# Kernel tuning notes

Hardware: AMD Instinct MI355X
Metric: run time of the kernel (lower is better)

## Reference

```python
import jax, jax.numpy as jnp
import numpy as np

N = 2500   # total_neurons
K = 50     # connections_per_neuron
T = 60     # temporal_sequence
F = 5      # input_features
H = 128    # lstm hidden_size
B = 512    # batch
GROUPS = [800, 700, 600, 400]  # support_resistance, trend_detection, pattern_recognition, volume_analysis


def _lstm_layer(x, Wih, Whh, bih, bhh):
    # x: [B, T, D]; PyTorch gate order (i, f, g, o); eval mode (no dropout)
    bs = x.shape[0]
    h0 = jnp.zeros((bs, H), x.dtype)

    def step(carry, xt):
        h, c = carry
        g = xt @ Wih.T + h @ Whh.T + bih + bhh
        i, f, gg, o = jnp.split(g, 4, axis=-1)
        c = jax.nn.sigmoid(f) * c + jax.nn.sigmoid(i) * jnp.tanh(gg)
        h = jax.nn.sigmoid(o) * jnp.tanh(c)
        return (h, c), h

    (h, c), ys = jax.lax.scan(step, (h0, h0), jnp.swapaxes(x, 0, 1))
    return jnp.swapaxes(ys, 0, 1), h


def _forward(x, W_ih0, W_hh0, b_ih0, b_hh0, W_ih1, W_hh1, b_ih1, b_hh1,
             fp_w1, fp_b1, fp_w2, fp_b2, conn_w, sens, thr,
             int_w1, int_b1, int_w2, int_b2, int_w3, int_b3,
             tw, tb, pw, pb, kw, kb, vw, vb, cw, cb, conn_idx):
    y0, _ = _lstm_layer(x, W_ih0, W_hh0, b_ih0, b_hh0)
    _, hlast = _lstm_layer(y0, W_ih1, W_hh1, b_ih1, b_hh1)        # hidden[-1]: [B, H]
    base = jnp.tanh(jax.nn.relu(hlast @ fp_w1.T + fp_b1) @ fp_w2.T + fp_b2)  # [B, 32]
    # all_activations = base repeated over N neurons; each neuron reduces its
    # K gathered activations (weighted) and the identical 32 feature dims to a scalar.
    feat_sum = base.sum(-1)                                        # [B]
    acts = jnp.broadcast_to(feat_sum[:, None], (x.shape[0], N))    # [B, N]
    gathered = acts[:, conn_idx]                                   # [B, N, K] irregular gather
    wi = jnp.einsum('bnk,nk->bn', gathered, conn_w)                # [B, N]
    pre = wi * sens
    o0 = GROUPS[0]; o1 = o0 + GROUPS[1]; o2 = o1 + GROUPS[2]
    neuron_out = jnp.concatenate([
        jax.nn.sigmoid(pre[:, :o0] - thr[:o0]),                    # support_resistance
        jnp.tanh(pre[:, o0:o1]),                                   # trend_detection
        jax.nn.relu(pre[:, o1:o2] - thr[o1:o2]),                   # pattern_recognition
        jax.nn.sigmoid(pre[:, o2:]),                               # volume_analysis
    ], axis=1)                                                     # [B, N]
    h1 = jax.nn.relu(neuron_out @ int_w1.T + int_b1)
    h2 = jax.nn.relu(h1 @ int_w2.T + int_b2)
    integrated = jnp.tanh(h2 @ int_w3.T + int_b3)                  # [B, 32]
    trend = integrated @ tw.T + tb                                 # [B, 3]
    patt = integrated @ pw.T + pb                                  # [B, 6]
    keyl = integrated @ kw.T + kb                                  # [B, 4]
    vol = integrated @ vw.T + vb                                   # [B, 1]
    conf = integrated @ cw.T + cb                                  # [B, 1]
    means = jnp.stack([neuron_out[:, :o0].mean(1), neuron_out[:, o0:o1].mean(1),
                       neuron_out[:, o1:o2].mean(1), neuron_out[:, o2:].mean(1)], axis=-1)
    # heads(15) + raw confidence(1) + overall_confidence(1) + specialty means(4) -> [B, 21]? no: 3+6+4+1+1+1+4 = 20
    return jnp.concatenate([trend, patt, keyl, vol, conf, jax.nn.sigmoid(conf), means], axis=-1)


def setup_inputs() -> dict:
    key = jax.random.key(0)
    ks = jax.random.split(key, 40)
    rn = lambda k, s, sc=0.1: jax.random.normal(k, s, dtype=jnp.float32) * sc
    inp = {}
    inp['x'] = jax.random.normal(ks[0], (B, T, F), dtype=jnp.float32)
    inp['W_ih0'] = rn(ks[1], (4 * H, F)); inp['W_hh0'] = rn(ks[2], (4 * H, H))
    inp['b_ih0'] = rn(ks[3], (4 * H,));   inp['b_hh0'] = rn(ks[4], (4 * H,))
    inp['W_ih1'] = rn(ks[5], (4 * H, H)); inp['W_hh1'] = rn(ks[6], (4 * H, H))
    inp['b_ih1'] = rn(ks[7], (4 * H,));   inp['b_hh1'] = rn(ks[8], (4 * H,))
    inp['fp_w1'] = rn(ks[9], (64, H));    inp['fp_b1'] = rn(ks[10], (64,))
    inp['fp_w2'] = rn(ks[11], (32, 64));  inp['fp_b2'] = rn(ks[12], (32,))
    inp['conn_w'] = rn(ks[13], (N, K))
    inp['sens'] = 1.0 + rn(ks[14], (N,))
    inp['thr'] = 0.6 + rn(ks[15], (N,))
    inp['int_w1'] = rn(ks[16], (256, N), 0.02); inp['int_b1'] = rn(ks[17], (256,))
    inp['int_w2'] = rn(ks[18], (64, 256));      inp['int_b2'] = rn(ks[19], (64,))
    inp['int_w3'] = rn(ks[20], (32, 64));       inp['int_b3'] = rn(ks[21], (32,))
    inp['tw'] = rn(ks[22], (3, 32)); inp['tb'] = rn(ks[23], (3,))
    inp['pw'] = rn(ks[24], (6, 32)); inp['pb'] = rn(ks[25], (6,))
    inp['kw'] = rn(ks[26], (4, 32)); inp['kb'] = rn(ks[27], (4,))
    inp['vw'] = rn(ks[28], (1, 32)); inp['vb'] = rn(ks[29], (1,))
    inp['cw'] = rn(ks[30], (1, 32)); inp['cb'] = rn(ks[31], (1,))
    inp['conn_idx'] = jax.random.randint(ks[32], (N, K), 0, N)
    return inp


def reference(x, W_ih0, W_hh0, b_ih0, b_hh0, W_ih1, W_hh1, b_ih1, b_hh1,
              fp_w1, fp_b1, fp_w2, fp_b2, conn_w, sens, thr,
              int_w1, int_b1, int_w2, int_b2, int_w3, int_b3,
              tw, tb, pw, pb, kw, kb, vw, vb, cw, cb, conn_idx):
    return _forward(x, W_ih0, W_hh0, b_ih0, b_hh0, W_ih1, W_hh1, b_ih1, b_hh1,
                    fp_w1, fp_b1, fp_w2, fp_b2, conn_w, sens, thr,
                    int_w1, int_b1, int_w2, int_b2, int_w3, int_b3,
                    tw, tb, pw, pb, kw, kb, vw, vb, cw, cb, conn_idx)
```

## Files before the change

### kernel.cpp

```cpp
#include <hip/hip_runtime.h>
#include <math.h>

#define NB   512
#define TT   60
#define FF   5
#define HH   128
#define G4   512
#define NN   2500
#define KK   50

#define O0 800
#define O1 1500
#define O2 2100

#define OFF_B0F   0
#define OFF_B1F   40960
#define OFF_XA    106496
#define OFF_BIAS0 598016
#define OFF_BIAS1 598528
#define OFF_A     599040
#define OFF_FS    601540
#define OFF_H1    602052

#define PREP_T0 81920
#define PREP_T1 212992
#define PREP_T2 1196032
#define PREP_T3 1196544
#define PREP_T4 1197056
#define PREP_TOTAL 1199556

typedef _Float16 f16x8 __attribute__((ext_vector_type(8)));
typedef float f32x4 __attribute__((ext_vector_type(4)));

__device__ __forceinline__ float sigf(float x) {
    return 1.0f / (1.0f + __expf(-x));
}
__device__ __forceinline__ float tanh2(float x) {
    float e = __expf(-2.0f * x);
    return fmaf(2.0f, 1.0f / (1.0f + e), -1.0f);
}

__global__ __launch_bounds__(256) void prep_kernel(
    const float* __restrict__ x,
    const float* __restrict__ W_ih0, const float* __restrict__ W_hh0,
    const float* __restrict__ b_ih0, const float* __restrict__ b_hh0,
    const float* __restrict__ W_ih1, const float* __restrict__ W_hh1,
    const float* __restrict__ b_ih1, const float* __restrict__ b_hh1,
    const float* __restrict__ conn_w, const float* __restrict__ sens,
    float* __restrict__ ws)
{
    int i = blockIdx.x * 256 + threadIdx.x;
    if (i >= PREP_TOTAL) return;

    if (i < PREP_T0) {
        int j = i & 7, l = (i >> 3) & 63;
        int rest = i >> 9;
        int g = rest & 3;
        int kbw = rest >> 2;
        int kb = kbw % 5, w = kbw / 5;
        int k = kb * 32 + (l >> 4) * 8 + j;
        int n = g * 128 + w * 16 + (l & 15);
        float val = 0.f;
        if (k < 128)       val = W_hh0[n * HH + k];
        else if (k < 133)  val = W_ih0[n * FF + (k - 128)];
        ((_Float16*)(ws + OFF_B0F))[i] = (_Float16)val;
    } else if (i < PREP_T1) {
        int v = i - PREP_T0;
        int j = v & 7, l = (v >> 3) & 63;
        int rest = v >> 9;
        int g = rest & 3;
        int kb = (rest >> 2) & 7;
        int w = rest >> 5;
        int k = kb * 32 + (l >> 4) * 8 + j;
        int n = g * 128 + w * 16 + (l & 15);
        float val = (k < 128) ? W_ih1[n * HH + k] : W_hh1[n * HH + (k - 128)];
        ((_Float16*)(ws + OFF_B1F))[v] = (_Float16)val;
    } else if (i < PREP_T2) {
        int v = i - PREP_T1;
        int j = v & 7, l = (v >> 3) & 63;
        int rest = v >> 9;
        int t = rest % 60, bb = rest / 60;
        float val = 0.f;
        if (l < 16 && j < 5)
            val = x[(bb * 16 + (l & 15)) * (TT * FF) + t * FF + j];
        ((_Float16*)(ws + OFF_XA))[v] = (_Float16)val;
    } else if (i < PREP_T3) {
        int j = i - PREP_T2;
        ws[OFF_BIAS0 + j] = b_ih0[j] + b_hh0[j];
    } else if (i < PREP_T4) {
        int j = i - PREP_T3;
        ws[OFF_BIAS1 + j] = b_ih1[j] + b_hh1[j];
    } else {
        int n = i - PREP_T4;
        float s = 0.f;
        const float* cw = conn_w + n * KK;
        for (int k = 0; k < KK; ++k) s += cw[k];
        ws[OFF_A + n] = s * sens[n];
    }
}

__global__ __launch_bounds__(512, 2) void lstm_mfma(
    const float* __restrict__ ws_ro,
    const float* __restrict__ fp_w1, const float* __restrict__ fp_b1,
    const float* __restrict__ fp_w2, const float* __restrict__ fp_b2,
    float* __restrict__ feat_sum)
{
    __shared__ __align__(16) _Float16 hcat[2 * 4096];
    __shared__ float t1s[16][65];
    __shared__ float bss[16][33];

    const int tid = threadIdx.x;
    const int w = tid >> 6, l = tid & 63;
    const int u = w * 16 + (l & 15);
    const int row0 = (l >> 4) * 4;
    const int bb = blockIdx.x;

    ((uint4*)hcat)[tid] = make_uint4(0u, 0u, 0u, 0u);

    float bia0[4], bia1[4];
#pragma unroll
    for (int g = 0; g < 4; ++g) {
        bia0[g] = ws_ro[OFF_BIAS0 + g * 128 + u];
        bia1[g] = ws_ro[OFF_BIAS1 + g * 128 + u];
    }
    float c0[4] = {0.f, 0.f, 0.f, 0.f};
    float c1[4] = {0.f, 0.f, 0.f, 0.f};

    const f16x8* B0 = (const f16x8*)(ws_ro + OFF_B0F) + w * 20 * 64 + l;
    const f16x8* B1 = (const f16x8*)(ws_ro + OFF_B1F) + w * 32 * 64 + l;
    const f16x8* XA = (const f16x8*)(ws_ro + OFF_XA) + bb * 60 * 64 + l;
    const f16x8* HF = (const f16x8*)hcat;

    f16x8 wb0[20];
#pragma unroll
    for (int i = 0; i < 20; ++i) wb0[i] = B0[i * 64];

    const int h0base = (u >> 5) * 512 + ((u >> 3) & 3) * 128 + (u & 7);
    const int h1base = h0base + 2048;

    f16x8 xa = XA[0];

    __syncthreads();

    auto step = [&](int SRC, int DST, int t) {
        const f16x8* hs = HF + SRC * 512;
        const f16x8* hd = HF + DST * 512;
        _Float16* hw = hcat + DST * 4096;

        f16x8 xan = XA[(t + 1 < TT ? t + 1 : TT - 1) * 64];

        f32x4 a0 = {0.f,0.f,0.f,0.f}, a1 = {0.f,0.f,0.f,0.f};
        f32x4 a2 = {0.f,0.f,0.f,0.f}, a3 = {0.f,0.f,0.f,0.f};
#pragma unroll
        for (int kb = 0; kb < 4; ++kb) {
            f16x8 af = hs[kb * 64 + l];
            a0 = __builtin_amdgcn_mfma_f32_16x16x32_f16(af, wb0[kb*4+0], a0, 0,0,0);
            a1 = __builtin_amdgcn_mfma_f32_16x16x32_f16(af, wb0[kb*4+1], a1, 0,0,0);
            a2 = __builtin_amdgcn_mfma_f32_16x16x32_f16(af, wb0[kb*4+2], a2, 0,0,0);
            a3 = __builtin_amdgcn_mfma_f32_16x16x32_f16(af, wb0[kb*4+3], a3, 0,0,0);
        }
        a0 = __builtin_amdgcn_mfma_f32_16x16x32_f16(xa, wb0[16], a0, 0,0,0);
        a1 = __builtin_amdgcn_mfma_f32_16x16x32_f16(xa, wb0[17], a1, 0,0,0);
        a2 = __builtin_amdgcn_mfma_f32_16x16x32_f16(xa, wb0[18], a2, 0,0,0);
        a3 = __builtin_amdgcn_mfma_f32_16x16x32_f16(xa, wb0[19], a3, 0,0,0);

        f16x8 q0 = B1[0*64], q1 = B1[1*64], q2 = B1[2*64], q3 = B1[3*64];

#pragma unroll
        for (int r = 0; r < 4; ++r) {
            float gi = sigf(a0[r] + bia0[0]);
            float gf = sigf(a1[r] + bia0[1]);
            float gg = tanh2(a2[r] + bia0[2]);
            float go = sigf(a3[r] + bia0[3]);
            c0[r] = gf * c0[r] + gi * gg;
            hw[h0base + (row0 + r) * 8] = (_Float16)(go * tanh2(c0[r]));
        }
        __syncthreads();

        f32x4 b0 = {0.f,0.f,0.f,0.f}, b1 = {0.f,0.f,0.f,0.f};
        f32x4 b2 = {0.f,0.f,0.f,0.f}, b3 = {0.f,0.f,0.f,0.f};
#pragma unroll
        for (int kb = 0; kb < 8; ++kb) {
            f16x8 af = (kb < 4) ? hd[kb * 64 + l] : hs[kb * 64 + l];
            f16x8 p0 = q0, p1 = q1, p2 = q2, p3 = q3;
            if (kb < 7) {
                q0 = B1[((kb+1)*4+0)*64]; q1 = B1[((kb+1)*4+1)*64];
                q2 = B1[((kb+1)*4+2)*64]; q3 = B1[((kb+1)*4+3)*64];
            }
            b0 = __builtin_amdgcn_mfma_f32_16x16x32_f16(af, p0, b0, 0,0,0);
            b1 = __builtin_amdgcn_mfma_f32_16x16x32_f16(af, p1, b1, 0,0,0);
            b2 = __builtin_amdgcn_mfma_f32_16x16x32_f16(af, p2, b2, 0,0,0);
            b3 = __builtin_amdgcn_mfma_f32_16x16x32_f16(af, p3, b3, 0,0,0);
        }
#pragma unroll
        for (int r = 0; r < 4; ++r) {
            float gi = sigf(b0[r] + bia1[0]);
            float gf = sigf(b1[r] + bia1[1]);
            float gg = tanh2(b2[r] + bia1[2]);
            float go = sigf(b3[r] + bia1[3]);
            c1[r] = gf * c1[r] + gi * gg;
            hw[h1base + (row0 + r) * 8] = (_Float16)(go * tanh2(c1[r]));
        }
        __syncthreads();
        xa = xan;
    };

    for (int t = 0; t < TT; t += 2) {
        step(0, 1, t);
        step(1, 0, t + 1);
    }

    for (int idx = tid; idx < 16 * 64; idx += 512) {
        int r = idx >> 6, m = idx & 63;
        float acc = fp_b1[m];
        const float* wp = fp_w1 + m * HH;
        for (int k = 0; k < HH; ++k) {
            float hv = (float)hcat[2048 + (k >> 5) * 512 +
                                   (r + ((k >> 3) & 3) * 16) * 8 + (k & 7)];
            acc = fmaf(wp[k], hv, acc);
        }
        t1s[r][m] = fmaxf(acc, 0.f);
    }
    __syncthreads();
    if (tid < 16 * 32) {
        int r = tid >> 5, q = tid & 31;
        float acc = fp_b2[q];
        const float* wp = fp_w2 + q * 64;
        for (int m = 0; m < 64; ++m) acc = fmaf(wp[m], t1s[r][m], acc);
        bss[r][q] = tanh2(acc);
    }
    __syncthreads();
    if (tid < 16) {
        float s = 0.f;
        for (int q = 0; q < 32; ++q) s += bss[tid][q];
        feat_sum[bb * 16 + tid] = s;
    }
}

__device__ __forceinline__ float actn(int n, float pre, float th) {
    if (n < O0)       return sigf(pre - th);
    else if (n < O1)  return tanh2(pre);
    else if (n < O2)  return fmaxf(pre - th, 0.f);
    else              return sigf(pre);
}

__global__ __launch_bounds__(256) void gemm_h1(
    const float* __restrict__ feat_sum,
    const float* __restrict__ aw, const float* __restrict__ thr,
    const float* __restrict__ int_w1,
    const float* __restrict__ int_b1,
    float* __restrict__ h1)
{
    __shared__ float As[32][33];
    __shared__ float Bs[32][33];
    const int b0 = blockIdx.x * 32;
    const int m0 = blockIdx.y * 32;
    const int tid = threadIdx.x;
    const int ty = tid >> 4, tx = tid & 15;
    const int li = tid >> 3;
    const int lj = (tid & 7) * 4;

    const float s_li = feat_sum[b0 + li];

    float acc00 = 0.f, acc01 = 0.f, acc10 = 0.f, acc11 = 0.f;

    for (int k0 = 0; k0 < NN; k0 += 32) {
        float4 av = make_float4(0.f, 0.f, 0.f, 0.f);
        if (k0 + lj < NN) {
            float4 aa = *(const float4*)(aw + k0 + lj);
            float4 tt = *(const float4*)(thr + k0 + lj);
            int n = k0 + lj;
            av.x = actn(n + 0, s_li * aa.x, tt.x);
            av.y = actn(n + 1, s_li * aa.y, tt.y);
            av.z = actn(n + 2, s_li * aa.z, tt.z);
            av.w = actn(n + 3, s_li * aa.w, tt.w);
        }
        As[li][lj + 0] = av.x; As[li][lj + 1] = av.y;
        As[li][lj + 2] = av.z; As[li][lj + 3] = av.w;

        float4 wv = make_float4(0.f, 0.f, 0.f, 0.f);
        if (k0 + lj < NN)
            wv = *(const float4*)(int_w1 + (m0 + li) * NN + k0 + lj);
        Bs[lj + 0][li] = wv.x; Bs[lj + 1][li] = wv.y;
        Bs[lj + 2][li] = wv.z; Bs[lj + 3][li] = wv.w;
        __syncthreads();

#pragma unroll 8
        for (int kk = 0; kk < 32; ++kk) {
            float a0 = As[ty * 2][kk],  a1 = As[ty * 2 + 1][kk];
            float w0 = Bs[kk][tx * 2],  w1 = Bs[kk][tx * 2 + 1];
            acc00 += a0 * w0; acc01 += a0 * w1;
            acc10 += a1 * w0; acc11 += a1 * w1;
        }
        __syncthreads();
    }
    const int bi = b0 + ty * 2, mj = m0 + tx * 2;
    h1[bi * 256 + mj]           = fmaxf(acc00 + int_b1[mj], 0.f);
    h1[bi * 256 + mj + 1]       = fmaxf(acc01 + int_b1[mj + 1], 0.f);
    h1[(bi + 1) * 256 + mj]     = fmaxf(acc10 + int_b1[mj], 0.f);
    h1[(bi + 1) * 256 + mj + 1] = fmaxf(acc11 + int_b1[mj + 1], 0.f);
}

__global__ __launch_bounds__(64) void tail_kernel(
    const float* __restrict__ h1,
    const float* __restrict__ feat_sum,
    const float* __restrict__ aw, const float* __restrict__ thr,
    const float* __restrict__ int_w2, const float* __restrict__ int_b2,
    const float* __restrict__ int_w3, const float* __restrict__ int_b3,
    const float* __restrict__ tw, const float* __restrict__ tb,
    const float* __restrict__ pw, const float* __restrict__ pb,
    const float* __restrict__ kw, const float* __restrict__ kb,
    const float* __restrict__ vw, const float* __restrict__ vb,
    const float* __restrict__ cw, const float* __restrict__ cb,
    float* __restrict__ out)
{
    const int b = blockIdx.x;
    const int lane = threadIdx.x;
    __shared__ float h2s[64];
    __shared__ float ints[32];
    __shared__ float outs[16];
    __shared__ float red[4][64];
    __shared__ float mred[4];

    {
        const float s = feat_sum[b];
        float m0 = 0.f, m1 = 0.f, m2 = 0.f, m3 = 0.f;
        for (int n = lane; n < NN; n += 64) {
            float v = actn(n, s * aw[n], thr[n]);
            if (n < O0) m0 += v; else if (n < O1) m1 += v;
            else if (n < O2) m2 += v; else m3 += v;
        }
        red[0][lane] = m0; red[1][lane] = m1;
        red[2][lane] = m2; red[3][lane] = m3;
    }

    {
        float acc = int_b2[lane];
        const float* hp = h1 + b * 256;
        const float* wp = int_w2 + lane * 256;
        for (int m = 0; m < 256; ++m) acc += wp[m] * hp[m];
        h2s[lane] = fmaxf(acc, 0.f);
    }
    __syncthreads();
    if (lane < 4) {
        float acc = 0.f;
        for (int i = 0; i < 64; ++i) acc += red[lane][i];
        const float inv[4] = {1.f/800.f, 1.f/700.f, 1.f/600.f, 1.f/400.f};
        mred[lane] = acc * inv[lane];
    }
    if (lane < 32) {
        float acc = int_b3[lane];
        const float* wp = int_w3 + lane * 64;
        for (int m = 0; m < 64; ++m) acc += wp[m] * h2s[m];
        ints[lane] = tanh2(acc);
    }
    __syncthreads();
    if (lane < 15) {
        const float* wsel; float bsel;
        if (lane < 3)       { wsel = tw + lane * 32;       bsel = tb[lane]; }
        else if (lane < 9)  { wsel = pw + (lane - 3) * 32; bsel = pb[lane - 3]; }
        else if (lane < 13) { wsel = kw + (lane - 9) * 32; bsel = kb[lane - 9]; }
        else if (lane == 13){ wsel = vw;                   bsel = vb[0]; }
        else                { wsel = cw;                   bsel = cb[0]; }
        float acc = bsel;
        for (int q = 0; q < 32; ++q) acc += wsel[q] * ints[q];
        outs[lane] = acc;
    }
    __syncthreads();
    if (lane < 20) {
        float v;
        if (lane < 15)       v = outs[lane];
        else if (lane == 15) v = sigf(outs[14]);
        else                 v = mred[lane - 16];
        out[b * 20 + lane] = v;
    }
}

extern "C" void kernel_launch(void* const* d_in, const int* in_sizes, int n_in,
                              void* d_out, int out_size, void* d_ws, size_t ws_size,
                              hipStream_t stream)
{
    const float* x      = (const float*)d_in[0];
    const float* W_ih0  = (const float*)d_in[1];
    const float* W_hh0  = (const float*)d_in[2];
    const float* b_ih0  = (const float*)d_in[3];
    const float* b_hh0  = (const float*)d_in[4];
    const float* W_ih1  = (const float*)d_in[5];
    const float* W_hh1  = (const float*)d_in[6];
    const float* b_ih1  = (const float*)d_in[7];
    const float* b_hh1  = (const float*)d_in[8];
    const float* fp_w1  = (const float*)d_in[9];
    const float* fp_b1  = (const float*)d_in[10];
    const float* fp_w2  = (const float*)d_in[11];
    const float* fp_b2  = (const float*)d_in[12];
    const float* conn_w = (const float*)d_in[13];
    const float* sens   = (const float*)d_in[14];
    const float* thr    = (const float*)d_in[15];
    const float* int_w1 = (const float*)d_in[16];
    const float* int_b1 = (const float*)d_in[17];
    const float* int_w2 = (const float*)d_in[18];
    const float* int_b2 = (const float*)d_in[19];
    const float* int_w3 = (const float*)d_in[20];
    const float* int_b3 = (const float*)d_in[21];
    const float* tw     = (const float*)d_in[22];
    const float* tb     = (const float*)d_in[23];
    const float* pw     = (const float*)d_in[24];
    const float* pb     = (const float*)d_in[25];
    const float* kw     = (const float*)d_in[26];
    const float* kb     = (const float*)d_in[27];
    const float* vw     = (const float*)d_in[28];
    const float* vb     = (const float*)d_in[29];
    const float* cw     = (const float*)d_in[30];
    const float* cb     = (const float*)d_in[31];

    float* ws = (float*)d_ws;
    float* out = (float*)d_out;

    prep_kernel<<<(PREP_TOTAL + 255) / 256, 256, 0, stream>>>(
        x, W_ih0, W_hh0, b_ih0, b_hh0, W_ih1, W_hh1, b_ih1, b_hh1,
        conn_w, sens, ws);

    lstm_mfma<<<NB / 16, 512, 0, stream>>>(
        ws, fp_w1, fp_b1, fp_w2, fp_b2, ws + OFF_FS);

    {
        dim3 grid(NB / 32, 256 / 32);
        gemm_h1<<<grid, 256, 0, stream>>>(
            ws + OFF_FS, ws + OFF_A, thr, int_w1, int_b1, ws + OFF_H1);
    }

    tail_kernel<<<NB, 64, 0, stream>>>(
        ws + OFF_H1, ws + OFF_FS, ws + OFF_A, thr,
        int_w2, int_b2, int_w3, int_b3,
        tw, tb, pw, pb, kw, kb, vw, vb, cw, cb,
        out);
}
```

Baseline: 428.4 us.

## Load input sequence into LDS inside LSTM kernel and drop prep staging

```diff
diff --git a/kernel.cpp b/kernel.cpp
--- a/kernel.cpp
+++ b/kernel.cpp
@@ -15,22 +15,22 @@
 
 #define OFF_B0F   0
 #define OFF_B1F   40960
-#define OFF_XA    106496
-#define OFF_BIAS0 598016
-#define OFF_BIAS1 598528
-#define OFF_A     599040
-#define OFF_FS    601540
-#define OFF_H1    602052
+#define OFF_BIAS0 106496
+#define OFF_BIAS1 107008
+#define OFF_A     107520
+#define OFF_FS    110020
+#define OFF_H1    110532
 
 #define PREP_T0 81920
 #define PREP_T1 212992
-#define PREP_T2 1196032
-#define PREP_T3 1196544
-#define PREP_T4 1197056
-#define PREP_TOTAL 1199556
+#define PREP_T2 213504
+#define PREP_T3 214016
+#define PREP_TOTAL 216516
 
 typedef _Float16 f16x8 __attribute__((ext_vector_type(8)));
 typedef float f32x4 __attribute__((ext_vector_type(4)));
+
+#define MFMA16(A, B, C) __builtin_amdgcn_mfma_f32_16x16x32_f16((A), (B), (C), 0, 0, 0)
 
 __device__ __forceinline__ float sigf(float x) {
     return 1.0f / (1.0f + __expf(-x));
@@ -41,7 +41,6 @@
 }
 
 __global__ __launch_bounds__(256) void prep_kernel(
-    const float* __restrict__ x,
     const float* __restrict__ W_ih0, const float* __restrict__ W_hh0,
     const float* __restrict__ b_ih0, const float* __restrict__ b_hh0,
     const float* __restrict__ W_ih1, const float* __restrict__ W_hh1,
@@ -76,22 +75,13 @@
         float val = (k < 128) ? W_ih1[n * HH + k] : W_hh1[n * HH + (k - 128)];
         ((_Float16*)(ws + OFF_B1F))[v] = (_Float16)val;
     } else if (i < PREP_T2) {
-        int v = i - PREP_T1;
-        int j = v & 7, l = (v >> 3) & 63;
-        int rest = v >> 9;
-        int t = rest % 60, bb = rest / 60;
-        float val = 0.f;
-        if (l < 16 && j < 5)
-            val = x[(bb * 16 + (l & 15)) * (TT * FF) + t * FF + j];
-        ((_Float16*)(ws + OFF_XA))[v] = (_Float16)val;
+        int j = i - PREP_T1;
+        ws[OFF_BIAS0 + j] = b_ih0[j] + b_hh0[j];
     } else if (i < PREP_T3) {
         int j = i - PREP_T2;
-        ws[OFF_BIAS0 + j] = b_ih0[j] + b_hh0[j];
-    } else if (i < PREP_T4) {
-        int j = i - PREP_T3;
         ws[OFF_BIAS1 + j] = b_ih1[j] + b_hh1[j];
     } else {
-        int n = i - PREP_T4;
+        int n = i - PREP_T3;
         float s = 0.f;
         const float* cw = conn_w + n * KK;
         for (int k = 0; k < KK; ++k) s += cw[k];
@@ -99,13 +89,15 @@
     }
 }
 
-__global__ __launch_bounds__(512, 2) void lstm_mfma(
+__global__ __launch_bounds__(512) void lstm_mfma(
+    const float* __restrict__ x,
     const float* __restrict__ ws_ro,
     const float* __restrict__ fp_w1, const float* __restrict__ fp_b1,
     const float* __restrict__ fp_w2, const float* __restrict__ fp_b2,
     float* __restrict__ feat_sum)
 {
     __shared__ __align__(16) _Float16 hcat[2 * 4096];
+    __shared__ _Float16 xsh[16][312];
     __shared__ float t1s[16][65];
     __shared__ float bss[16][33];
 
@@ -117,6 +109,11 @@
 
     ((uint4*)hcat)[tid] = make_uint4(0u, 0u, 0u, 0u);
 
+    for (int i = tid; i < 16 * TT * FF; i += 512) {
+        int r = i / (TT * FF), c = i % (TT * FF);
+        xsh[r][c] = (_Float16)x[(bb * 16 + r) * (TT * FF) + c];
+    }
+
     float bia0[4], bia1[4];
 #pragma unroll
     for (int g = 0; g < 4; ++g) {
@@ -128,17 +125,10 @@
 
     const f16x8* B0 = (const f16x8*)(ws_ro + OFF_B0F) + w * 20 * 64 + l;
     const f16x8* B1 = (const f16x8*)(ws_ro + OFF_B1F) + w * 32 * 64 + l;
-    const f16x8* XA = (const f16x8*)(ws_ro + OFF_XA) + bb * 60 * 64 + l;
     const f16x8* HF = (const f16x8*)hcat;
-
-    f16x8 wb0[20];
-#pragma unroll
-    for (int i = 0; i < 20; ++i) wb0[i] = B0[i * 64];
 
     const int h0base = (u >> 5) * 512 + ((u >> 3) & 3) * 128 + (u & 7);
     const int h1base = h0base + 2048;
-
-    f16x8 xa = XA[0];
 
     __syncthreads();
 
@@ -147,62 +137,64 @@
         const f16x8* hd = HF + DST * 512;
         _Float16* hw = hcat + DST * 4096;
 
-        f16x8 xan = XA[(t + 1 < TT ? t + 1 : TT - 1) * 64];
-
-        f32x4 a0 = {0.f,0.f,0.f,0.f}, a1 = {0.f,0.f,0.f,0.f};
-        f32x4 a2 = {0.f,0.f,0.f,0.f}, a3 = {0.f,0.f,0.f,0.f};
+        f16x8 xaf = {(_Float16)0, (_Float16)0, (_Float16)0, (_Float16)0,
+                     (_Float16)0, (_Float16)0, (_Float16)0, (_Float16)0};
+        if (l < 16) {
+            const _Float16* xr = &xsh[l][t * FF];
+            xaf[0] = xr[0]; xaf[1] = xr[1]; xaf[2] = xr[2];
+            xaf[3] = xr[3]; xaf[4] = xr[4];
+        }
+
+        f32x4 a0 = {bia0[0], bia0[0], bia0[0], bia0[0]};
+        f32x4 a1 = {bia0[1], bia0[1], bia0[1], bia0[1]};
+        f32x4 a2 = {bia0[2], bia0[2], bia0[2], bia0[2]};
+        f32x4 a3 = {bia0[3], bia0[3], bia0[3], bia0[3]};
 #pragma unroll
         for (int kb = 0; kb < 4; ++kb) {
             f16x8 af = hs[kb * 64 + l];
-            a0 = __builtin_amdgcn_mfma_f32_16x16x32_f16(af, wb0[kb*4+0], a0, 0,0,0);
-            a1 = __builtin_amdgcn_mfma_f32_16x16x32_f16(af, wb0[kb*4+1], a1, 0,0,0);
-            a2 = __builtin_amdgcn_mfma_f32_16x16x32_f16(af, wb0[kb*4+2], a2, 0,0,0);
-            a3 = __builtin_amdgcn_mfma_f32_16x16x32_f16(af, wb0[kb*4+3], a3, 0,0,0);
-        }
-        a0 = __builtin_amdgcn_mfma_f32_16x16x32_f16(xa, wb0[16], a0, 0,0,0);
-        a1 = __builtin_amdgcn_mfma_f32_16x16x32_f16(xa, wb0[17], a1, 0,0,0);
-        a2 = __builtin_amdgcn_mfma_f32_16x16x32_f16(xa, wb0[18], a2, 0,0,0);
-        a3 = __builtin_amdgcn_mfma_f32_16x16x32_f16(xa, wb0[19], a3, 0,0,0);
-
-        f16x8 q0 = B1[0*64], q1 = B1[1*64], q2 = B1[2*64], q3 = B1[3*64];
+            a0 = MFMA16(af, B0[(kb*4+0)*64], a0);
+            a1 = MFMA16(af, B0[(kb*4+1)*64], a1);
+            a2 = MFMA16(af, B0[(kb*4+2)*64], a2);
+            a3 = MFMA16(af, B0[(kb*4+3)*64], a3);
+        }
+        a0 = MFMA16(xaf, B0[(16+0)*64], a0);
+        a1 = MFMA16(xaf, B0[(16+1)*64], a1);
+        a2 = MFMA16(xaf, B0[(16+2)*64], a2);
+        a3 = MFMA16(xaf, B0[(16+3)*64], a3);
 
 #pragma unroll
         for (int r = 0; r < 4; ++r) {
-            float gi = sigf(a0[r] + bia0[0]);
-            float gf = sigf(a1[r] + bia0[1]);
-            float gg = tanh2(a2[r] + bia0[2]);
-            float go = sigf(a3[r] + bia0[3]);
+            float gi = sigf(a0[r]);
+            float gf = sigf(a1[r]);
+            float gg = tanh2(a2[r]);
+            float go = sigf(a3[r]);
             c0[r] = gf * c0[r] + gi * gg;
             hw[h0base + (row0 + r) * 8] = (_Float16)(go * tanh2(c0[r]));
         }
         __syncthreads();
 
-        f32x4 b0 = {0.f,0.f,0.f,0.f}, b1 = {0.f,0.f,0.f,0.f};
-        f32x4 b2 = {0.f,0.f,0.f,0.f}, b3 = {0.f,0.f,0.f,0.f};
+        f32x4 b0 = {bia1[0], bia1[0], bia1[0], bia1[0]};
+        f32x4 b1 = {bia1[1], bia1[1], bia1[1], bia1[1]};
+        f32x4 b2 = {bia1[2], bia1[2], bia1[2], bia1[2]};
+        f32x4 b3 = {bia1[3], bia1[3], bia1[3], bia1[3]};
 #pragma unroll
         for (int kb = 0; kb < 8; ++kb) {
             f16x8 af = (kb < 4) ? hd[kb * 64 + l] : hs[kb * 64 + l];
-            f16x8 p0 = q0, p1 = q1, p2 = q2, p3 = q3;
-            if (kb < 7) {
-                q0 = B1[((kb+1)*4+0)*64]; q1 = B1[((kb+1)*4+1)*64];
-                q2 = B1[((kb+1)*4+2)*64]; q3 = B1[((kb+1)*4+3)*64];
-            }
-            b0 = __builtin_amdgcn_mfma_f32_16x16x32_f16(af, p0, b0, 0,0,0);
-            b1 = __builtin_amdgcn_mfma_f32_16x16x32_f16(af, p1, b1, 0,0,0);
-            b2 = __builtin_amdgcn_mfma_f32_16x16x32_f16(af, p2, b2, 0,0,0);
-            b3 = __builtin_amdgcn_mfma_f32_16x16x32_f16(af, p3, b3, 0,0,0);
+            b0 = MFMA16(af, B1[(kb*4+0)*64], b0);
+            b1 = MFMA16(af, B1[(kb*4+1)*64], b1);
+            b2 = MFMA16(af, B1[(kb*4+2)*64], b2);
+            b3 = MFMA16(af, B1[(kb*4+3)*64], b3);
         }
 #pragma unroll
         for (int r = 0; r < 4; ++r) {
-            float gi = sigf(b0[r] + bia1[0]);
-            float gf = sigf(b1[r] + bia1[1]);
-            float gg = tanh2(b2[r] + bia1[2]);
-            float go = sigf(b3[r] + bia1[3]);
+            float gi = sigf(b0[r]);
+            float gf = sigf(b1[r]);
+            float gg = tanh2(b2[r]);
+            float go = sigf(b3[r]);
             c1[r] = gf * c1[r] + gi * gg;
             hw[h1base + (row0 + r) * 8] = (_Float16)(go * tanh2(c1[r]));
         }
         __syncthreads();
-        xa = xan;
     };
 
     for (int t = 0; t < TT; t += 2) {
@@ -417,11 +409,11 @@
     float* out = (float*)d_out;
 
     prep_kernel<<<(PREP_TOTAL + 255) / 256, 256, 0, stream>>>(
-        x, W_ih0, W_hh0, b_ih0, b_hh0, W_ih1, W_hh1, b_ih1, b_hh1,
+        W_ih0, W_hh0, b_ih0, b_hh0, W_ih1, W_hh1, b_ih1, b_hh1,
         conn_w, sens, ws);
 
     lstm_mfma<<<NB / 16, 512, 0, stream>>>(
-        ws, fp_w1, fp_b1, fp_w2, fp_b2, ws + OFF_FS);
+        x, ws, fp_w1, fp_b1, fp_w2, fp_b2, ws + OFF_FS);
 
     {
         dim3 grid(NB / 32, 256 / 32);
```

Result: slower. 451.7 us (+5.4%).
